# Performance work log

Hardware: AMD Instinct MI355X
Metric: run time of the kernel (lower is better)

The kernel has to match this reference:

```python
import jax, jax.numpy as jnp
import numpy as np
import math

DIM = 1024
NUM_HEADS = 16
HEAD_DIM = DIM // NUM_HEADS
LOGIT_SCALE_MAX = math.log(1.0 / 0.01)
EPS = 1e-12  # F.normalize eps


def setup_inputs() -> dict:
    key = jax.random.key(0)
    ks = jax.random.split(key, 4)
    L, N, C = 1024, 8, DIM
    scale = HEAD_DIM ** -0.5
    x = jax.random.normal(ks[0], (L, N, C), dtype=jnp.float32)
    in_proj_weight = jax.random.normal(ks[1], (3 * C, C), dtype=jnp.float32) * scale
    in_proj_bias = jnp.zeros((3 * C,), dtype=jnp.float32)
    logit_scale = jnp.full((NUM_HEADS, 1, 1), math.log(10.0), dtype=jnp.float32)
    head_scale = jnp.ones((NUM_HEADS, 1, 1), dtype=jnp.float32)
    out_w = jax.random.normal(ks[2], (C, C), dtype=jnp.float32) * (C ** -0.5)
    out_b = jax.random.normal(ks[3], (C,), dtype=jnp.float32) * 0.01
    return {"x": x, "in_proj_weight": in_proj_weight, "in_proj_bias": in_proj_bias,
            "logit_scale": logit_scale, "head_scale": head_scale,
            "out_w": out_w, "out_b": out_b}


def _l2_normalize(t):
    # matches F.normalize(t, dim=-1): t / max(||t||_2, eps)
    n = jnp.sqrt(jnp.sum(t * t, axis=-1, keepdims=True))
    return t / jnp.maximum(n, EPS)


def reference(x, in_proj_weight, in_proj_bias, logit_scale, head_scale, out_w, out_b):
    L, N, C = x.shape
    H, hd = NUM_HEADS, HEAD_DIM
    qkv = x @ in_proj_weight.T + in_proj_bias          # (L, N, 3C)
    q, k, v = jnp.split(qkv, 3, axis=-1)               # each (L, N, C)

    def to_heads(t):  # (L, N, C) -> (N, H, L, hd)
        return t.reshape(L, N, H, hd).transpose(1, 2, 0, 3)

    q, k, v = to_heads(q), to_heads(k), to_heads(v)
    # scaled-cosine attention
    ls = jnp.exp(jnp.minimum(logit_scale, LOGIT_SCALE_MAX))  # (H,1,1) broadcasts
    attn = jnp.einsum('nhld,nhmd->nhlm', _l2_normalize(q), _l2_normalize(k)) * ls
    attn = jax.nn.softmax(attn, axis=-1)               # (N, H, L, L)
    o = jnp.einsum('nhlm,nhmd->nhld', attn, v)         # (N, H, L, hd)
    o = o * head_scale                                  # per-head scale
    o = o.transpose(2, 0, 1, 3).reshape(L, N, C)       # back to (L, N, C)
    return o @ out_w.T + out_b
```

## Files before the change

kernel.cpp:

```cpp
#include <hip/hip_runtime.h>
#include <hip/hip_bf16.h>

typedef __hip_bfloat16 bf16;
typedef __attribute__((ext_vector_type(8))) short bf16x8;
typedef __attribute__((ext_vector_type(4))) float f32x4;

#define LOGIT_MAX 4.6051702f

__device__ __forceinline__ float4 load4(const float* p) { return *(const float4*)p; }

__device__ __forceinline__ void store4bf(bf16* p, float4 v) {
    union { bf16 b[4]; uint2 u; } t;
    t.b[0] = __float2bfloat16(v.x); t.b[1] = __float2bfloat16(v.y);
    t.b[2] = __float2bfloat16(v.z); t.b[3] = __float2bfloat16(v.w);
    *(uint2*)p = t.u;
}

__device__ __forceinline__ void async16(const bf16* g, const bf16* lds) {
    __builtin_amdgcn_global_load_lds(
        (const __attribute__((address_space(1))) void*)g,
        (__attribute__((address_space(3))) void*)lds, 16, 0, 0);
}

__global__ __launch_bounds__(256) void prep_kernel(
    const void* __restrict__ x, const void* __restrict__ w_in, const void* __restrict__ out_w,
    const void* __restrict__ b_in, const void* __restrict__ out_b,
    const void* __restrict__ ls, const void* __restrict__ hs,
    bf16* __restrict__ xb, bf16* __restrict__ wb, bf16* __restrict__ owb,
    float* __restrict__ smallf, int* __restrict__ flag)
{
    __shared__ int cnt_lds[4];
    const unsigned short* xs = (const unsigned short*)x;
    int c = 0;
    for (int i = threadIdx.x; i < 4096; i += 256) {
        const unsigned e = (xs[i] >> 7) & 0xFF;
        if (e >= 0x90) c++;
    }
#pragma unroll
    for (int off = 32; off > 0; off >>= 1) c += __shfl_down(c, off, 64);
    if ((threadIdx.x & 63) == 0) cnt_lds[threadIdx.x >> 6] = c;
    __syncthreads();
    const int f = (cnt_lds[0] + cnt_lds[1] + cnt_lds[2] + cnt_lds[3] > 64) ? 1 : 0;

    if (blockIdx.x == 0) {
        if (threadIdx.x == 0) *flag = f;
        for (int idx = threadIdx.x; idx < 4128; idx += 256) {
            float v;
            if (f) {
                if (idx < 3072)      v = ((const float*)b_in)[idx];
                else if (idx < 4096) v = ((const float*)out_b)[idx - 3072];
                else if (idx < 4112) v = expf(fminf(((const float*)ls)[idx - 4096], LOGIT_MAX));
                else                 v = ((const float*)hs)[idx - 4112];
            } else {
                if (idx < 3072)      v = __bfloat162float(((const bf16*)b_in)[idx]);
                else if (idx < 4096) v = __bfloat162float(((const bf16*)out_b)[idx - 3072]);
                else if (idx < 4112) v = expf(fminf(__bfloat162float(((const bf16*)ls)[idx - 4096]), LOGIT_MAX));
                else                 v = __bfloat162float(((const bf16*)hs)[idx - 4112]);
            }
            smallf[idx] = v;
        }
    }
    if (f != 1) return;
    const size_t NX = 8388608, NW = 3145728, NO = 1048576;
    const size_t t0   = ((size_t)blockIdx.x * 256 + threadIdx.x) * 4;
    const size_t step = (size_t)gridDim.x * 256 * 4;
    for (size_t i = t0; i < NX; i += step) store4bf(xb + i, load4((const float*)x + i));
    for (size_t i = t0; i < NW; i += step) store4bf(wb + i, load4((const float*)w_in + i));
    for (size_t i = t0; i < NO; i += step) store4bf(owb + i, load4((const float*)out_w + i));
}

__global__ __launch_bounds__(256, 4) void qkv_gemm_mfma_kernel(
    const int* __restrict__ flag,
    const bf16* __restrict__ Xws, const bf16* __restrict__ Wws,
    const bf16* __restrict__ Xdir, const bf16* __restrict__ Wdir,
    const float* __restrict__ bias_f,
    bf16* __restrict__ q, bf16* __restrict__ k, bf16* __restrict__ vt)
{
    const bf16* X = (*flag) ? Xws : Xdir;
    const bf16* W = (*flag) ? Wws : Wdir;
    __shared__ bf16 A_lds[128 * 64];
    __shared__ bf16 B_lds[128 * 64];
    const int tid  = threadIdx.x;
    const int w    = tid >> 6;
    const int lane = tid & 63;
    const int l16  = lane & 15, quad = lane >> 4;
    const int wm   = w >> 1, wn = w & 1;
    const int row0 = blockIdx.y * 128;
    const int col0 = blockIdx.x * 128;
    const int sr   = lane >> 3, sc = lane & 7;
    const int scg  = sc ^ sr;

    f32x4 acc[4][4] = {};

    for (int kt = 0; kt < 1024; kt += 64) {
        __syncthreads();
#pragma unroll
        for (int i = 0; i < 4; i++) {
            const int br = w * 32 + i * 8;
            async16(X + (size_t)(row0 + br + sr) * 1024 + kt + scg * 8, &A_lds[br * 64]);
            async16(W + (size_t)(col0 + br + sr) * 1024 + kt + scg * 8, &B_lds[br * 64]);
        }
        __syncthreads();

#pragma unroll
        for (int kh = 0; kh < 2; kh++) {
            bf16x8 af[4], bf[4];
#pragma unroll
            for (int mt = 0; mt < 4; mt++) {
                const int row = wm * 64 + mt * 16 + l16;
                af[mt] = *(const bf16x8*)&A_lds[row * 64 + (((quad + kh * 4) ^ (row & 7)) * 8)];
            }
#pragma unroll
            for (int nt = 0; nt < 4; nt++) {
                const int row = wn * 64 + nt * 16 + l16;
                bf[nt] = *(const bf16x8*)&B_lds[row * 64 + (((quad + kh * 4) ^ (row & 7)) * 8)];
            }
#pragma unroll
            for (int mt = 0; mt < 4; mt++)
#pragma unroll
                for (int nt = 0; nt < 4; nt++)
                    acc[mt][nt] = __builtin_amdgcn_mfma_f32_16x16x32_bf16(af[mt], bf[nt], acc[mt][nt], 0, 0, 0);
        }
    }

    const int cbase = col0 + wn * 64;
    const int part  = cbase >> 10;
    const int h     = (cbase & 1023) >> 6;
    float bias[4];
#pragma unroll
    for (int nt = 0; nt < 4; nt++) bias[nt] = bias_f[cbase + nt * 16 + l16];

    if (part < 2) {
        bf16* dst0 = (part == 0) ? q : k;
#pragma unroll
        for (int mt = 0; mt < 4; mt++) {
#pragma unroll
            for (int rg = 0; rg < 4; rg++) {
                const int r = row0 + wm * 64 + mt * 16 + quad * 4 + rg;
                const int l = r >> 3, nn = r & 7;
                float val[4]; float ss = 0.f;
#pragma unroll
                for (int nt = 0; nt < 4; nt++) {
                    val[nt] = acc[mt][nt][rg] + bias[nt];
                    ss += val[nt] * val[nt];
                }
                ss += __shfl_xor(ss, 1); ss += __shfl_xor(ss, 2);
                ss += __shfl_xor(ss, 4); ss += __shfl_xor(ss, 8);
                const float inv = 1.f / fmaxf(sqrtf(ss), 1e-12f);
                bf16* dp = dst0 + ((size_t)((nn * 16 + h) * 1024 + l)) * 64;
#pragma unroll
                for (int nt = 0; nt < 4; nt++)
                    dp[nt * 16 + l16] = __float2bfloat16(val[nt] * inv);
            }
        }
    } else {
#pragma unroll
        for (int mt = 0; mt < 4; mt++) {
#pragma unroll
            for (int rg = 0; rg < 4; rg++) {
                const int r = row0 + wm * 64 + mt * 16 + quad * 4 + rg;
                const int l = r >> 3, nn = r & 7;
#pragma unroll
                for (int nt = 0; nt < 4; nt++) {
                    const int d = nt * 16 + l16;
                    vt[((size_t)((nn * 16 + h) * 64 + d)) * 1024 + l] =
                        __float2bfloat16(acc[mt][nt][rg] + bias[nt]);
                }
            }
        }
    }
}

__global__ __launch_bounds__(256, 2) void attn_mfma_kernel(
    const bf16* __restrict__ q, const bf16* __restrict__ k,
    const bf16* __restrict__ vt, const float* __restrict__ scale_f,
    bf16* __restrict__ o)
{
    __shared__ bf16 K_lds[64][64];
    __shared__ bf16 Vt_lds[64][64];
    __shared__ bf16 P_lds[4][64][72];
    __shared__ float l_lds[4][64];

    const int bid  = blockIdx.x;
    const int qt   = bid >> 7;
    const int nh   = bid & 127;
    const int h    = nh & 15;
    const int n    = nh >> 4;
    const int tid  = threadIdx.x;
    const int w    = tid >> 6;
    const int lane = tid & 63;
    const int l16  = lane & 15;
    const int quad = lane >> 4;

    const size_t base = (size_t)nh * (1024 * 64);
    const float ls   = scale_f[4096 + h];
    const float hs   = scale_f[4112 + h];
    const float lsl2 = ls * 1.4426950408889634f;

    bf16x8 qf[4][2];
#pragma unroll
    for (int u = 0; u < 4; u++) {
        const int qrow = qt * 256 + w * 64 + u * 16 + l16;
        const bf16* qp = q + base + (size_t)qrow * 64 + quad * 8;
        qf[u][0] = *(const bf16x8*)qp;
        qf[u][1] = *(const bf16x8*)(qp + 32);
    }

    f32x4 o_acc[4][4] = {};
    float l_part[4] = {};

    const int sr = lane >> 3;
    const int sc = lane & 7;

    for (int j0 = 0; j0 < 1024; j0 += 64) {
        __syncthreads();
#pragma unroll
        for (int half = 0; half < 2; half++) {
            const int br  = w * 16 + half * 8;
            const int row = br + sr;
            const int cg  = sc ^ (row & 7);
            async16(k  + base + (size_t)(j0 + row) * 64 + cg * 8, &K_lds[br][0]);
            async16(vt + base + (size_t)row * 1024 + j0 + cg * 8, &Vt_lds[br][0]);
        }
        __syncthreads();

        bf16x8 kf[4][2];
#pragma unroll
        for (int s = 0; s < 4; s++) {
            const int krow = s * 16 + l16;
            const int swz  = krow & 7;
            kf[s][0] = *(const bf16x8*)&K_lds[krow][(quad ^ swz) * 8];
            kf[s][1] = *(const bf16x8*)&K_lds[krow][((quad + 4) ^ swz) * 8];
        }

#pragma unroll
        for (int u = 0; u < 4; u++) {
#pragma unroll
            for (int s = 0; s < 4; s++) {
                f32x4 a = {};
                a = __builtin_amdgcn_mfma_f32_16x16x32_bf16(kf[s][0], qf[u][0], a, 0, 0, 0);
                a = __builtin_amdgcn_mfma_f32_16x16x32_bf16(kf[s][1], qf[u][1], a, 0, 0, 0);
                union { bf16 b[4]; uint2 uu; } pk;
                float sum = 0.f;
#pragma unroll
                for (int r = 0; r < 4; r++) {
                    const float p = exp2f(fmaf(a[r], lsl2, -lsl2));
                    pk.b[r] = __float2bfloat16(p);
                    sum += p;
                }
                l_part[u] += sum;
                *(uint2*)&P_lds[w][u * 16 + l16][s * 16 + quad * 4] = pk.uu;
            }
        }

        bf16x8 pf[4][2];
#pragma unroll
        for (int u = 0; u < 4; u++) {
            pf[u][0] = *(const bf16x8*)&P_lds[w][u * 16 + l16][quad * 8];
            pf[u][1] = *(const bf16x8*)&P_lds[w][u * 16 + l16][32 + quad * 8];
        }
#pragma unroll
        for (int ds = 0; ds < 4; ds++) {
            const int vrow = ds * 16 + l16;
            const int swz  = vrow & 7;
            const bf16x8 vf0 = *(const bf16x8*)&Vt_lds[vrow][(quad ^ swz) * 8];
            const bf16x8 vf1 = *(const bf16x8*)&Vt_lds[vrow][((quad + 4) ^ swz) * 8];
#pragma unroll
            for (int u = 0; u < 4; u++) {
                o_acc[u][ds] = __builtin_amdgcn_mfma_f32_16x16x32_bf16(pf[u][0], vf0, o_acc[u][ds], 0, 0, 0);
                o_acc[u][ds] = __builtin_amdgcn_mfma_f32_16x16x32_bf16(pf[u][1], vf1, o_acc[u][ds], 0, 0, 0);
            }
        }
    }

#pragma unroll
    for (int u = 0; u < 4; u++) {
        float v = l_part[u];
        v += __shfl_xor(v, 16);
        v += __shfl_xor(v, 32);
        l_lds[w][u * 16 + l16] = v;
    }

#pragma unroll
    for (int u = 0; u < 4; u++) {
#pragma unroll
        for (int r = 0; r < 4; r++) {
            const float inv = hs / l_lds[w][u * 16 + quad * 4 + r];
            const int row_l = qt * 256 + w * 64 + u * 16 + quad * 4 + r;
            bf16* dst = o + ((size_t)row_l * 8 + n) * 1024 + h * 64 + l16;
#pragma unroll
            for (int ds = 0; ds < 4; ds++)
                dst[ds * 16] = __float2bfloat16(o_acc[u][ds][r] * inv);
        }
    }
}

__global__ __launch_bounds__(256, 4) void out_gemm_mfma_kernel(
    const int* __restrict__ flag,
    const bf16* __restrict__ A,
    const bf16* __restrict__ Bws, const bf16* __restrict__ Bdir,
    const float* __restrict__ bias_f,
    float* __restrict__ outf, bf16* __restrict__ outb)
{
    const int f = *flag;
    const bf16* B = f ? Bws : Bdir;
    __shared__ bf16 A_lds[128 * 64];
    __shared__ bf16 B_lds[128 * 64];
    const int tid  = threadIdx.x;
    const int w    = tid >> 6;
    const int lane = tid & 63;
    const int l16  = lane & 15, quad = lane >> 4;
    const int wm   = w >> 1, wn = w & 1;
    const int row0 = blockIdx.y * 128;
    const int col0 = blockIdx.x * 128;
    const int sr   = lane >> 3, sc = lane & 7;
    const int scg  = sc ^ sr;

    f32x4 acc[4][4] = {};

    for (int kt = 0; kt < 1024; kt += 64) {
        __syncthreads();
#pragma unroll
        for (int i = 0; i < 4; i++) {
            const int br = w * 32 + i * 8;
            async16(A + (size_t)(row0 + br + sr) * 1024 + kt + scg * 8, &A_lds[br * 64]);
            async16(B + (size_t)(col0 + br + sr) * 1024 + kt + scg * 8, &B_lds[br * 64]);
        }
        __syncthreads();

#pragma unroll
        for (int kh = 0; kh < 2; kh++) {
            bf16x8 af[4], bf[4];
#pragma unroll
            for (int mt = 0; mt < 4; mt++) {
                const int row = wm * 64 + mt * 16 + l16;
                af[mt] = *(const bf16x8*)&A_lds[row * 64 + (((quad + kh * 4) ^ (row & 7)) * 8)];
            }
#pragma unroll
            for (int nt = 0; nt < 4; nt++) {
                const int row = wn * 64 + nt * 16 + l16;
                bf[nt] = *(const bf16x8*)&B_lds[row * 64 + (((quad + kh * 4) ^ (row & 7)) * 8)];
            }
#pragma unroll
            for (int mt = 0; mt < 4; mt++)
#pragma unroll
                for (int nt = 0; nt < 4; nt++)
                    acc[mt][nt] = __builtin_amdgcn_mfma_f32_16x16x32_bf16(af[mt], bf[nt], acc[mt][nt], 0, 0, 0);
        }
    }

#pragma unroll
    for (int mt = 0; mt < 4; mt++) {
        const int rbase = row0 + wm * 64 + mt * 16 + quad * 4;
#pragma unroll
        for (int nt = 0; nt < 4; nt++) {
            const int c = col0 + wn * 64 + nt * 16 + l16;
            const float bias = bias_f[c];
#pragma unroll
            for (int rg = 0; rg < 4; rg++) {
                const float v = acc[mt][nt][rg] + bias;
                const size_t idx = (size_t)(rbase + rg) * 1024 + c;
                if (f) outf[idx] = v; else outb[idx] = __float2bfloat16(v);
            }
        }
    }
}

extern "C" void kernel_launch(void* const* d_in, const int* in_sizes, int n_in,
                              void* d_out, int out_size, void* d_ws, size_t ws_size,
                              hipStream_t stream)
{
    const size_t SEG = (size_t)8 * 16 * 1024 * 64;
    bf16* qn  = (bf16*)d_ws;
    bf16* kn  = qn + SEG;
    bf16* vt  = kn + SEG;
    bf16* ow  = vt + SEG;
    bf16* xb  = ow + SEG;
    bf16* wb  = xb + SEG;
    bf16* owb = wb + 3145728;
    float* smallf = (float*)(owb + 1048576);
    int*   flag   = (int*)(smallf + 4128);

    prep_kernel<<<2048, 256, 0, stream>>>(
        d_in[0], d_in[1], d_in[5], d_in[2], d_in[6], d_in[3], d_in[4],
        xb, wb, owb, smallf, flag);

    qkv_gemm_mfma_kernel<<<dim3(3072 / 128, 8192 / 128), 256, 0, stream>>>(
        flag, xb, wb, (const bf16*)d_in[0], (const bf16*)d_in[1], smallf, qn, kn, vt);

    attn_mfma_kernel<<<dim3(128 * 4), 256, 0, stream>>>(qn, kn, vt, smallf, ow);

    out_gemm_mfma_kernel<<<dim3(1024 / 128, 8192 / 128), 256, 0, stream>>>(
        flag, ow, owb, (const bf16*)d_in[5], smallf + 3072,
        (float*)d_out, (bf16*)d_out);
}
```

Before: 280.5 us.

## Double-buffer K/V tiles in attention and enlarge QKV GEMM row tile

The attention kernel now keeps two K and V^T LDS buffers and issues the async loads for the next 64-key tile before computing on the current one. This is meant to hide global-load latency behind the MFMA and softmax work. Separately, the QKV GEMM block tile grows from 128x128 to 256x128: each wave holds 8x4 accumulators and each B fragment is reused across twice as many rows, with launch bounds relaxed to 2 blocks per CU. The cost is more LDS and registers, so occupancy drops, and the GEMM grid shrinks to 768 blocks. The overlap may also be lost if the compiler places a full wait for outstanding loads before the LDS reads.

```diff
diff --git a/kernel.cpp b/kernel.cpp
--- a/kernel.cpp
+++ b/kernel.cpp
@@ -69,7 +69,7 @@
     for (size_t i = t0; i < NO; i += step) store4bf(owb + i, load4((const float*)out_w + i));
 }
 
-__global__ __launch_bounds__(256, 4) void qkv_gemm_mfma_kernel(
+__global__ __launch_bounds__(256, 2) void qkv_gemm_mfma_kernel(
     const int* __restrict__ flag,
     const bf16* __restrict__ Xws, const bf16* __restrict__ Wws,
     const bf16* __restrict__ Xdir, const bf16* __restrict__ Wdir,
@@ -78,48 +78,50 @@
 {
     const bf16* X = (*flag) ? Xws : Xdir;
     const bf16* W = (*flag) ? Wws : Wdir;
-    __shared__ bf16 A_lds[128 * 64];
+    __shared__ bf16 A_lds[256 * 64];
     __shared__ bf16 B_lds[128 * 64];
     const int tid  = threadIdx.x;
     const int w    = tid >> 6;
     const int lane = tid & 63;
     const int l16  = lane & 15, quad = lane >> 4;
     const int wm   = w >> 1, wn = w & 1;
-    const int row0 = blockIdx.y * 128;
+    const int row0 = blockIdx.y * 256;
     const int col0 = blockIdx.x * 128;
     const int sr   = lane >> 3, sc = lane & 7;
     const int scg  = sc ^ sr;
 
-    f32x4 acc[4][4] = {};
+    f32x4 acc[8][4] = {};
 
     for (int kt = 0; kt < 1024; kt += 64) {
         __syncthreads();
 #pragma unroll
+        for (int i = 0; i < 8; i++) {
+            const int br = w * 64 + i * 8;
+            async16(X + (size_t)(row0 + br + sr) * 1024 + kt + scg * 8, &A_lds[br * 64]);
+        }
+#pragma unroll
         for (int i = 0; i < 4; i++) {
             const int br = w * 32 + i * 8;
-            async16(X + (size_t)(row0 + br + sr) * 1024 + kt + scg * 8, &A_lds[br * 64]);
             async16(W + (size_t)(col0 + br + sr) * 1024 + kt + scg * 8, &B_lds[br * 64]);
         }
         __syncthreads();
 
 #pragma unroll
         for (int kh = 0; kh < 2; kh++) {
-            bf16x8 af[4], bf[4];
-#pragma unroll
-            for (int mt = 0; mt < 4; mt++) {
-                const int row = wm * 64 + mt * 16 + l16;
-                af[mt] = *(const bf16x8*)&A_lds[row * 64 + (((quad + kh * 4) ^ (row & 7)) * 8)];
-            }
+            bf16x8 bf[4];
 #pragma unroll
             for (int nt = 0; nt < 4; nt++) {
                 const int row = wn * 64 + nt * 16 + l16;
                 bf[nt] = *(const bf16x8*)&B_lds[row * 64 + (((quad + kh * 4) ^ (row & 7)) * 8)];
             }
 #pragma unroll
-            for (int mt = 0; mt < 4; mt++)
+            for (int mt = 0; mt < 8; mt++) {
+                const int row = wm * 128 + mt * 16 + l16;
+                const bf16x8 af = *(const bf16x8*)&A_lds[row * 64 + (((quad + kh * 4) ^ (row & 7)) * 8)];
 #pragma unroll
                 for (int nt = 0; nt < 4; nt++)
-                    acc[mt][nt] = __builtin_amdgcn_mfma_f32_16x16x32_bf16(af[mt], bf[nt], acc[mt][nt], 0, 0, 0);
+                    acc[mt][nt] = __builtin_amdgcn_mfma_f32_16x16x32_bf16(af, bf[nt], acc[mt][nt], 0, 0, 0);
+            }
         }
     }
 
@@ -133,10 +135,10 @@
     if (part < 2) {
         bf16* dst0 = (part == 0) ? q : k;
 #pragma unroll
-        for (int mt = 0; mt < 4; mt++) {
+        for (int mt = 0; mt < 8; mt++) {
 #pragma unroll
             for (int rg = 0; rg < 4; rg++) {
-                const int r = row0 + wm * 64 + mt * 16 + quad * 4 + rg;
+                const int r = row0 + wm * 128 + mt * 16 + quad * 4 + rg;
                 const int l = r >> 3, nn = r & 7;
                 float val[4]; float ss = 0.f;
 #pragma unroll
@@ -155,10 +157,10 @@
         }
     } else {
 #pragma unroll
-        for (int mt = 0; mt < 4; mt++) {
+        for (int mt = 0; mt < 8; mt++) {
 #pragma unroll
             for (int rg = 0; rg < 4; rg++) {
-                const int r = row0 + wm * 64 + mt * 16 + quad * 4 + rg;
+                const int r = row0 + wm * 128 + mt * 16 + quad * 4 + rg;
                 const int l = r >> 3, nn = r & 7;
 #pragma unroll
                 for (int nt = 0; nt < 4; nt++) {
@@ -176,8 +178,8 @@
     const bf16* __restrict__ vt, const float* __restrict__ scale_f,
     bf16* __restrict__ o)
 {
-    __shared__ bf16 K_lds[64][64];
-    __shared__ bf16 Vt_lds[64][64];
+    __shared__ bf16 K_lds[2][64][64];
+    __shared__ bf16 Vt_lds[2][64][64];
     __shared__ bf16 P_lds[4][64][72];
     __shared__ float l_lds[4][64];
 
@@ -212,25 +214,31 @@
     const int sr = lane >> 3;
     const int sc = lane & 7;
 
-    for (int j0 = 0; j0 < 1024; j0 += 64) {
-        __syncthreads();
+    auto stage = [&](int j0, int b) {
 #pragma unroll
         for (int half = 0; half < 2; half++) {
             const int br  = w * 16 + half * 8;
             const int row = br + sr;
             const int cg  = sc ^ (row & 7);
-            async16(k  + base + (size_t)(j0 + row) * 64 + cg * 8, &K_lds[br][0]);
-            async16(vt + base + (size_t)row * 1024 + j0 + cg * 8, &Vt_lds[br][0]);
-        }
+            async16(k  + base + (size_t)(j0 + row) * 64 + cg * 8, &K_lds[b][br][0]);
+            async16(vt + base + (size_t)row * 1024 + j0 + cg * 8, &Vt_lds[b][br][0]);
+        }
+    };
+
+    stage(0, 0);
+
+    for (int jt = 0; jt < 16; jt++) {
+        const int cur = jt & 1;
         __syncthreads();
+        if (jt < 15) stage((jt + 1) * 64, cur ^ 1);
 
         bf16x8 kf[4][2];
 #pragma unroll
         for (int s = 0; s < 4; s++) {
             const int krow = s * 16 + l16;
             const int swz  = krow & 7;
-            kf[s][0] = *(const bf16x8*)&K_lds[krow][(quad ^ swz) * 8];
-            kf[s][1] = *(const bf16x8*)&K_lds[krow][((quad + 4) ^ swz) * 8];
+            kf[s][0] = *(const bf16x8*)&K_lds[cur][krow][(quad ^ swz) * 8];
+            kf[s][1] = *(const bf16x8*)&K_lds[cur][krow][((quad + 4) ^ swz) * 8];
         }
 
 #pragma unroll
@@ -263,8 +271,8 @@
         for (int ds = 0; ds < 4; ds++) {
             const int vrow = ds * 16 + l16;
             const int swz  = vrow & 7;
-            const bf16x8 vf0 = *(const bf16x8*)&Vt_lds[vrow][(quad ^ swz) * 8];
-            const bf16x8 vf1 = *(const bf16x8*)&Vt_lds[vrow][((quad + 4) ^ swz) * 8];
+            const bf16x8 vf0 = *(const bf16x8*)&Vt_lds[cur][vrow][(quad ^ swz) * 8];
+            const bf16x8 vf1 = *(const bf16x8*)&Vt_lds[cur][vrow][((quad + 4) ^ swz) * 8];
 #pragma unroll
             for (int u = 0; u < 4; u++) {
                 o_acc[u][ds] = __builtin_amdgcn_mfma_f32_16x16x32_bf16(pf[u][0], vf0, o_acc[u][ds], 0, 0, 0);
@@ -385,7 +393,7 @@
         d_in[0], d_in[1], d_in[5], d_in[2], d_in[6], d_in[3], d_in[4],
         xb, wb, owb, smallf, flag);
 
-    qkv_gemm_mfma_kernel<<<dim3(3072 / 128, 8192 / 128), 256, 0, stream>>>(
+    qkv_gemm_mfma_kernel<<<dim3(3072 / 128, 8192 / 256), 256, 0, stream>>>(
         flag, xb, wb, (const bf16*)d_in[0], (const bf16*)d_in[1], smallf, qn, kn, vt);
 
     attn_mfma_kernel<<<dim3(128 * 4), 256, 0, stream>>>(qn, kn, vt, smallf, ow);
```

New measurement: 293.3 us. 4.6% more time.
